# Kernel optimization log

Measured on AMD Instinct MI355X. Metric: run time of the kernel, lower is better.

Reference implementation:

```python
import jax, jax.numpy as jnp
import numpy as np


def setup_inputs() -> dict:
    key = jax.random.key(0)
    ks = jax.random.split(key, 7)
    N, D, H1, H2, M = 16384, 2048, 512, 32, 2048
    return {
        "x": jax.random.normal(ks[0], (N, D), dtype=jnp.float32),
        "W1": jax.random.normal(ks[1], (H1, D), dtype=jnp.float32) * (1.0 / np.sqrt(D)),
        "b1": jax.random.normal(ks[2], (H1,), dtype=jnp.float32) * 0.01,
        "W2": jax.random.normal(ks[3], (H2, H1), dtype=jnp.float32) * (1.0 / np.sqrt(H1)),
        "b2": jax.random.normal(ks[4], (H2,), dtype=jnp.float32) * 0.01,
        "a_memory": jax.random.normal(ks[5], (M, H2), dtype=jnp.float32),
        "n_memory": jax.random.normal(ks[6], (M, H2), dtype=jnp.float32),
    }


def reference(x, W1, b1, W2, b2, a_memory, n_memory):
    # MLP per forward(): linear -> relu -> (dropout p=0) -> linear -> (dropout p=0)
    h = jax.nn.relu(x @ W1.T + b1)          # [N, 512]
    feat = h @ W2.T + b2                     # [N, 32] (no ReLU in forward path)
    inv_d = 1.0 / feat.shape[1]
    # caption_score(mem, f) = max_j mean(mem_j * f) = max_j (mem_j . f) / 32
    a_score = jnp.max(feat @ a_memory.T, axis=1) * inv_d  # [N]
    n_score = jnp.max(feat @ n_memory.T, axis=1) * inv_d  # [N]
    return jax.nn.sigmoid(a_score - n_score)
```

## Files before the change

kernel.cpp:

```cpp
#include <hip/hip_runtime.h>
#include <hip/hip_bf16.h>

typedef __attribute__((ext_vector_type(8))) __bf16 bf16x8;
typedef __attribute__((ext_vector_type(4))) float f32x4;

#define NROWS 16384
#define DIM   2048
#define NH1   512
#define NH2   32
#define MMEM  2048
#define BK    32
#define NT    (DIM / BK)

#define W1O ((size_t)0)
#define W2O ((size_t)2097152)
#define AMO ((size_t)2129920)
#define NMO ((size_t)2260992)
#define HO  ((size_t)2392064)

__device__ __forceinline__ f32x4 mfma16(bf16x8 a, bf16x8 b, f32x4 c) {
    return __builtin_amdgcn_mfma_f32_16x16x32_bf16(a, b, c, 0, 0, 0);
}

__device__ __forceinline__ void gload_lds16(const void* g, void* l) {
    __builtin_amdgcn_global_load_lds(
        (const __attribute__((address_space(1))) void*)g,
        (__attribute__((address_space(3))) void*)l, 16, 0, 0);
}

__device__ __forceinline__ bf16x8 cvt8(f32x4 a, f32x4 b) {
    bf16x8 o;
    o[0] = (__bf16)a[0]; o[1] = (__bf16)a[1]; o[2] = (__bf16)a[2]; o[3] = (__bf16)a[3];
    o[4] = (__bf16)b[0]; o[5] = (__bf16)b[1]; o[6] = (__bf16)b[2]; o[7] = (__bf16)b[3];
    return o;
}

struct bf4 { __bf16 a, b, c, d; };

__global__ void cvt_all_kernel(const float* __restrict__ w1f, __bf16* __restrict__ w1b,
                               const float* __restrict__ w2f, __bf16* __restrict__ w2b,
                               const float* __restrict__ amf, __bf16* __restrict__ amb,
                               const float* __restrict__ nmf, __bf16* __restrict__ nmb) {
    const int g = blockIdx.x * blockDim.x + threadIdx.x;
    const int T = gridDim.x * blockDim.x;
    for (int i = g; i < (NH1 * DIM) / 4; i += T) {
        const float4 v = *reinterpret_cast<const float4*>(w1f + i * 4);
        *reinterpret_cast<bf4*>(w1b + i * 4) = { (__bf16)v.x, (__bf16)v.y, (__bf16)v.z, (__bf16)v.w };
    }
    for (int i = g; i < (NH2 * NH1) / 4; i += T) {
        const float4 v = *reinterpret_cast<const float4*>(w2f + i * 4);
        *reinterpret_cast<bf4*>(w2b + i * 4) = { (__bf16)v.x, (__bf16)v.y, (__bf16)v.z, (__bf16)v.w };
    }
    for (int i = g; i < (MMEM * NH2) / 4; i += T) {
        const float4 v = *reinterpret_cast<const float4*>(amf + i * 4);
        *reinterpret_cast<bf4*>(amb + i * 4) = { (__bf16)v.x, (__bf16)v.y, (__bf16)v.z, (__bf16)v.w };
    }
    for (int i = g; i < (MMEM * NH2) / 4; i += T) {
        const float4 v = *reinterpret_cast<const float4*>(nmf + i * 4);
        *reinterpret_cast<bf4*>(nmb + i * 4) = { (__bf16)v.x, (__bf16)v.y, (__bf16)v.z, (__bf16)v.w };
    }
}

__global__ __launch_bounds__(256, 2) void gemm1_kernel(
    const float*  __restrict__ Xf,
    const __bf16* __restrict__ W1,
    const float*  __restrict__ b1,
    __bf16* __restrict__ Hout)
{
    __shared__ float  As[3][128 * BK];
    __shared__ __bf16 Bs[4][128 * BK];
    const int tid  = threadIdx.x;
    const int lane = tid & 63;
    const int wave = tid >> 6;
    const int b = blockIdx.x;
    const int orig = (b & 7) * 64 + (b >> 3);
    const int bn = orig & 3;
    const int bm = orig >> 2;
    const size_t brow = (size_t)bm * 128;
    const int bcol = bn * 128;
    const int wr = wave >> 1, wc = wave & 1;

    f32x4 acc[4][4];
#pragma unroll
    for (int m = 0; m < 4; ++m)
#pragma unroll
        for (int n = 0; n < 4; ++n) acc[m][n] = (f32x4){0.f, 0.f, 0.f, 0.f};

    const int aRowT = tid >> 3;
    const int cA    = (tid & 7) ^ (aRowT & 7);
    const float* aSrcBase = Xf + (brow + aRowT) * (size_t)DIM + cA * 4;
    const int bRowT = tid >> 2;
    const int cB    = (tid & 3) ^ ((tid >> 3) & 3);
    const __bf16* bSrcBase = W1 + (size_t)(bcol + bRowT) * DIM + cB * 8;

#define STAGE_A(T, BI)                                                        \
    {                                                                         \
        const int k0_ = (T) * BK;                                             \
        _Pragma("unroll")                                                     \
        for (int q = 0; q < 4; ++q)                                           \
            gload_lds16(aSrcBase + (size_t)q * 32 * DIM + k0_,                \
                        (char*)As[BI] + q * 4096 + tid * 16);                 \
    }
#define STAGE_B(T, BI)                                                        \
    {                                                                         \
        const int k0_ = (T) * BK;                                             \
        _Pragma("unroll")                                                     \
        for (int q = 0; q < 2; ++q)                                           \
            gload_lds16(bSrcBase + (size_t)q * 64 * DIM + k0_,                \
                        (char*)Bs[BI] + q * 4096 + tid * 16);                 \
    }

    const int l15 = lane & 15;
    const int kc  = lane >> 4;
    const int l7  = lane & 7;
    const int rABase = wr * 64 + l15;
    const int rBBase = wc * 64 + l15;
    const int aSlot0 = ((2 * kc)     ^ l7) << 4;
    const int aSlot1 = ((2 * kc + 1) ^ l7) << 4;
    const int bSlot  = (kc ^ ((l15 >> 1) & 3)) << 4;

#define COMPUTE(AI, BI)                                                       \
    {                                                                         \
        const char* Ac = (const char*)As[AI];                                 \
        const char* Bc = (const char*)Bs[BI];                                 \
        bf16x8 av[4], bv[4];                                                  \
        _Pragma("unroll")                                                     \
        for (int m = 0; m < 4; ++m) {                                         \
            const int rowB = (rABase + m * 16) * 128;                         \
            f32x4 lo = *(const f32x4*)(Ac + rowB + aSlot0);                   \
            f32x4 hi = *(const f32x4*)(Ac + rowB + aSlot1);                   \
            av[m] = cvt8(lo, hi);                                             \
        }                                                                     \
        _Pragma("unroll")                                                     \
        for (int n = 0; n < 4; ++n)                                           \
            bv[n] = *(const bf16x8*)(Bc + (rBBase + n * 16) * 64 + bSlot);    \
        __builtin_amdgcn_s_setprio(1);                                        \
        _Pragma("unroll")                                                     \
        for (int m = 0; m < 4; ++m)                                           \
            _Pragma("unroll")                                                 \
            for (int n = 0; n < 4; ++n)                                       \
                acc[m][n] = mfma16(av[m], bv[n], acc[m][n]);                  \
        __builtin_amdgcn_s_setprio(0);                                        \
    }

    STAGE_A(0, 0);
    STAGE_B(0, 0);
    STAGE_A(1, 1);
    STAGE_B(1, 1);
    STAGE_B(2, 2);

    int ia = 0;
    int i2 = 2;
    for (int t = 0; t < NT; ++t) {
        asm volatile("s_waitcnt vmcnt(8)" ::: "memory");
        __builtin_amdgcn_s_barrier();
        __builtin_amdgcn_sched_barrier(0);
        const int tA = (t + 2 < NT) ? (t + 2) : (NT - 1);
        const int tB = (t + 3 < NT) ? (t + 3) : (NT - 1);
        STAGE_A(tA, i2);
        STAGE_B(tB, (t + 3) & 3);
        __builtin_amdgcn_sched_barrier(0);
        COMPUTE(ia, t & 3);
        ia = (ia == 2) ? 0 : ia + 1;
        i2 = (i2 == 2) ? 0 : i2 + 1;
    }
#undef STAGE_A
#undef STAGE_B
#undef COMPUTE

#pragma unroll
    for (int n = 0; n < 4; ++n) {
        const int gcol = bcol + wc * 64 + n * 16 + l15;
        const float bias = b1[gcol];
#pragma unroll
        for (int m = 0; m < 4; ++m) {
            const size_t grow0 = brow + wr * 64 + m * 16 + kc * 4;
#pragma unroll
            for (int r = 0; r < 4; ++r) {
                float v = acc[m][n][r] + bias;
                v = v > 0.f ? v : 0.f;
                Hout[(grow0 + r) * NH1 + gcol] = (__bf16)v;
            }
        }
    }
}

__global__ __launch_bounds__(512) void tail_kernel(
    const __bf16* __restrict__ Hin,
    const __bf16* __restrict__ W2b,
    const float*  __restrict__ b2,
    const __bf16* __restrict__ Am,
    const __bf16* __restrict__ Nm,
    float* __restrict__ out)
{
    __shared__ __bf16 featLds[64 * 32];
    __shared__ float aMaxLds[2][64];
    __shared__ float nMaxLds[2][64];
    const int tid  = threadIdx.x;
    const int lane = tid & 63;
    const int wave = tid >> 6;
    const int rowBase = blockIdx.x * 64;
    const int l15 = lane & 15;
    const int kc  = lane >> 4;
    const int rgrp  = (wave & 3) * 16;
    const int jHalf = wave >> 2;

    if (wave < 4) {
        f32x4 acc0 = {0.f,0.f,0.f,0.f}, acc1 = {0.f,0.f,0.f,0.f};
        const size_t hrow = (size_t)(rowBase + rgrp + l15) * NH1;
#pragma unroll
        for (int kk = 0; kk < 16; ++kk) {
            bf16x8 a  = *(const bf16x8*)(Hin + hrow + kk * 32 + kc * 8);
            bf16x8 w0 = *(const bf16x8*)(W2b + (size_t)l15 * NH1 + kk * 32 + kc * 8);
            bf16x8 w1 = *(const bf16x8*)(W2b + (size_t)(16 + l15) * NH1 + kk * 32 + kc * 8);
            acc0 = mfma16(a, w0, acc0);
            acc1 = mfma16(a, w1, acc1);
        }
        const float bias0 = b2[l15], bias1 = b2[16 + l15];
#pragma unroll
        for (int r = 0; r < 4; ++r) {
            const int lr = rgrp + kc * 4 + r;
            featLds[lr * 32 + l15]      = (__bf16)(acc0[r] + bias0);
            featLds[lr * 32 + 16 + l15] = (__bf16)(acc1[r] + bias1);
        }
    }
    __syncthreads();

    const bf16x8 af = *(const bf16x8*)&featLds[(rgrp + l15) * 32 + kc * 8];

    float rmaxA[4], rmaxN[4];
#pragma unroll
    for (int r = 0; r < 4; ++r) { rmaxA[r] = -1e30f; rmaxN[r] = -1e30f; }
    const f32x4 zero = {0.f,0.f,0.f,0.f};
    const int jBase = jHalf * (MMEM / 2);
#pragma unroll 2
    for (int jt = 0; jt < (MMEM / 2) / 16; jt += 4) {
        bf16x8 ba[4], bb[4];
#pragma unroll
        for (int u = 0; u < 4; ++u) {
            const size_t off = (size_t)(jBase + (jt + u) * 16 + l15) * NH2 + kc * 8;
            ba[u] = *(const bf16x8*)(Am + off);
            bb[u] = *(const bf16x8*)(Nm + off);
        }
#pragma unroll
        for (int u = 0; u < 4; ++u) {
            f32x4 sa = mfma16(af, ba[u], zero);
            f32x4 sn = mfma16(af, bb[u], zero);
#pragma unroll
            for (int r = 0; r < 4; ++r) {
                rmaxA[r] = fmaxf(rmaxA[r], sa[r]);
                rmaxN[r] = fmaxf(rmaxN[r], sn[r]);
            }
        }
    }
#pragma unroll
    for (int off = 1; off < 16; off <<= 1) {
#pragma unroll
        for (int r = 0; r < 4; ++r) {
            rmaxA[r] = fmaxf(rmaxA[r], __shfl_xor(rmaxA[r], off, 64));
            rmaxN[r] = fmaxf(rmaxN[r], __shfl_xor(rmaxN[r], off, 64));
        }
    }
    if (l15 == 0) {
#pragma unroll
        for (int r = 0; r < 4; ++r) {
            const int row = rgrp + kc * 4 + r;
            aMaxLds[jHalf][row] = rmaxA[r];
            nMaxLds[jHalf][row] = rmaxN[r];
        }
    }
    __syncthreads();
    if (tid < 64) {
        const float ma = fmaxf(aMaxLds[0][tid], aMaxLds[1][tid]);
        const float mn = fmaxf(nMaxLds[0][tid], nMaxLds[1][tid]);
        const float d = (ma - mn) * (1.0f / 32.0f);
        out[rowBase + tid] = 1.0f / (1.0f + __expf(-d));
    }
}

extern "C" void kernel_launch(void* const* d_in, const int* in_sizes, int n_in,
                              void* d_out, int out_size, void* d_ws, size_t ws_size,
                              hipStream_t stream) {
    (void)in_sizes; (void)n_in; (void)out_size; (void)ws_size;
    const float* x  = (const float*)d_in[0];
    const float* W1 = (const float*)d_in[1];
    const float* b1 = (const float*)d_in[2];
    const float* W2 = (const float*)d_in[3];
    const float* b2 = (const float*)d_in[4];
    const float* am = (const float*)d_in[5];
    const float* nm = (const float*)d_in[6];
    float* out = (float*)d_out;
    char* ws = (char*)d_ws;
    __bf16* w1b = (__bf16*)(ws + W1O);
    __bf16* w2b = (__bf16*)(ws + W2O);
    __bf16* amb = (__bf16*)(ws + AMO);
    __bf16* nmb = (__bf16*)(ws + NMO);
    __bf16* hb  = (__bf16*)(ws + HO);

    cvt_all_kernel<<<dim3(512), dim3(256), 0, stream>>>(W1, w1b, W2, w2b, am, amb, nm, nmb);
    gemm1_kernel<<<dim3((NROWS / 128) * (NH1 / 128)), dim3(256), 0, stream>>>(x, w1b, b1, hb);
    tail_kernel<<<dim3(NROWS / 64), dim3(512), 0, stream>>>(hb, w2b, b2, amb, nmb, out);
}
```

Baseline: 91.73 us.

## Load W1 tiles directly into registers, dropping B LDS staging and raising occupancy

The B operand (bf16 W1) is no longer staged through shared memory. Each wave now loads its MFMA B fragments straight from global memory into registers, double-buffered across a 2x-unrolled K loop. This frees the Bs LDS allocation so the launch bound can rise from 2 to 3 blocks per CU, and it removes the LDS reads for B. In exchange, global B loads are repeated per wave, since the wr waves sharing a column block each load the same data, and the vmcnt accounting now mixes register and LDS loads, which risks stalls or hazards.

```diff
diff --git a/kernel.cpp b/kernel.cpp
--- a/kernel.cpp
+++ b/kernel.cpp
@@ -61,14 +61,13 @@
     }
 }
 
-__global__ __launch_bounds__(256, 2) void gemm1_kernel(
+__global__ __launch_bounds__(256, 3) void gemm1_kernel(
     const float*  __restrict__ Xf,
     const __bf16* __restrict__ W1,
     const float*  __restrict__ b1,
     __bf16* __restrict__ Hout)
 {
-    __shared__ float  As[3][128 * BK];
-    __shared__ __bf16 Bs[4][128 * BK];
+    __shared__ float As[3][128 * BK];
     const int tid  = threadIdx.x;
     const int lane = tid & 63;
     const int wave = tid >> 6;
@@ -89,9 +88,6 @@
     const int aRowT = tid >> 3;
     const int cA    = (tid & 7) ^ (aRowT & 7);
     const float* aSrcBase = Xf + (brow + aRowT) * (size_t)DIM + cA * 4;
-    const int bRowT = tid >> 2;
-    const int cB    = (tid & 3) ^ ((tid >> 3) & 3);
-    const __bf16* bSrcBase = W1 + (size_t)(bcol + bRowT) * DIM + cB * 8;
 
 #define STAGE_A(T, BI)                                                        \
     {                                                                         \
@@ -101,71 +97,76 @@
             gload_lds16(aSrcBase + (size_t)q * 32 * DIM + k0_,                \
                         (char*)As[BI] + q * 4096 + tid * 16);                 \
     }
-#define STAGE_B(T, BI)                                                        \
-    {                                                                         \
-        const int k0_ = (T) * BK;                                             \
-        _Pragma("unroll")                                                     \
-        for (int q = 0; q < 2; ++q)                                           \
-            gload_lds16(bSrcBase + (size_t)q * 64 * DIM + k0_,                \
-                        (char*)Bs[BI] + q * 4096 + tid * 16);                 \
-    }
 
     const int l15 = lane & 15;
     const int kc  = lane >> 4;
     const int l7  = lane & 7;
+    const __bf16* bBase = W1 + (size_t)(bcol + wc * 64 + l15) * DIM + kc * 8;
+
+#define LOAD_BV(T, DST)                                                       \
+    {                                                                         \
+        _Pragma("unroll")                                                     \
+        for (int n = 0; n < 4; ++n)                                           \
+            DST[n] = *(const bf16x8*)(bBase + (size_t)(n * 16) * DIM + (T) * BK); \
+    }
+
     const int rABase = wr * 64 + l15;
-    const int rBBase = wc * 64 + l15;
     const int aSlot0 = ((2 * kc)     ^ l7) << 4;
     const int aSlot1 = ((2 * kc + 1) ^ l7) << 4;
-    const int bSlot  = (kc ^ ((l15 >> 1) & 3)) << 4;
-
-#define COMPUTE(AI, BI)                                                       \
+
+#define COMPUTE(BI, BV)                                                       \
     {                                                                         \
-        const char* Ac = (const char*)As[AI];                                 \
-        const char* Bc = (const char*)Bs[BI];                                 \
-        bf16x8 av[4], bv[4];                                                  \
+        const char* Ac = (const char*)As[BI];                                 \
+        bf16x8 av[4];                                                         \
         _Pragma("unroll")                                                     \
         for (int m = 0; m < 4; ++m) {                                         \
-            const int rowB = (rABase + m * 16) * 128;                         \
-            f32x4 lo = *(const f32x4*)(Ac + rowB + aSlot0);                   \
-            f32x4 hi = *(const f32x4*)(Ac + rowB + aSlot1);                   \
+            const char* rp = Ac + (rABase + m * 16) * 128;                    \
+            f32x4 lo = *(const f32x4*)(rp + aSlot0);                          \
+            f32x4 hi = *(const f32x4*)(rp + aSlot1);                          \
             av[m] = cvt8(lo, hi);                                             \
         }                                                                     \
-        _Pragma("unroll")                                                     \
-        for (int n = 0; n < 4; ++n)                                           \
-            bv[n] = *(const bf16x8*)(Bc + (rBBase + n * 16) * 64 + bSlot);    \
         __builtin_amdgcn_s_setprio(1);                                        \
         _Pragma("unroll")                                                     \
         for (int m = 0; m < 4; ++m)                                           \
             _Pragma("unroll")                                                 \
             for (int n = 0; n < 4; ++n)                                       \
-                acc[m][n] = mfma16(av[m], bv[n], acc[m][n]);                  \
+                acc[m][n] = mfma16(av[m], BV[n], acc[m][n]);                  \
         __builtin_amdgcn_s_setprio(0);                                        \
     }
 
+    bf16x8 bva[4], bvb[4];
+
     STAGE_A(0, 0);
-    STAGE_B(0, 0);
     STAGE_A(1, 1);
-    STAGE_B(1, 1);
-    STAGE_B(2, 2);
-
-    int ia = 0;
-    int i2 = 2;
-    for (int t = 0; t < NT; ++t) {
+    LOAD_BV(0, bva);
+
+#pragma unroll 1
+    for (int t = 0; t < NT; t += 2) {
         asm volatile("s_waitcnt vmcnt(8)" ::: "memory");
         __builtin_amdgcn_s_barrier();
         __builtin_amdgcn_sched_barrier(0);
-        const int tA = (t + 2 < NT) ? (t + 2) : (NT - 1);
-        const int tB = (t + 3 < NT) ? (t + 3) : (NT - 1);
-        STAGE_A(tA, i2);
-        STAGE_B(tB, (t + 3) & 3);
-        __builtin_amdgcn_sched_barrier(0);
-        COMPUTE(ia, t & 3);
-        ia = (ia == 2) ? 0 : ia + 1;
-        i2 = (i2 == 2) ? 0 : i2 + 1;
+        LOAD_BV(t + 1, bvb);
+        __builtin_amdgcn_sched_barrier(0);
+        COMPUTE(t % 3, bva);
+        __builtin_amdgcn_sched_barrier(0);
+        {
+            const int tA = (t + 2 < NT) ? (t + 2) : (NT - 1);
+            STAGE_A(tA, (t + 2) % 3);
+        }
+        asm volatile("s_waitcnt vmcnt(8)" ::: "memory");
+        __builtin_amdgcn_s_barrier();
+        __builtin_amdgcn_sched_barrier(0);
+        if (t + 2 < NT) LOAD_BV(t + 2, bva);
+        __builtin_amdgcn_sched_barrier(0);
+        COMPUTE((t + 1) % 3, bvb);
+        __builtin_amdgcn_sched_barrier(0);
+        {
+            const int tA = (t + 3 < NT) ? (t + 3) : (NT - 1);
+            STAGE_A(tA, (t + 3) % 3);
+        }
     }
 #undef STAGE_A
-#undef STAGE_B
+#undef LOAD_BV
 #undef COMPUTE
 
 #pragma unroll
```

After: 111.1 us. +21.1%, slower.
